# Optimization experiments

Hardware: AMD Instinct MI355X
Metric: run time of the kernel (lower is better)

The kernel has to match this reference:

```python
import jax, jax.numpy as jnp
import numpy as np

B, N, H, D, DEPTH = 16, 1024, 2, 128, 3
A = H * D  # atten_dim = 256
FFN = 1024
EPS = 1e-5


def layer_norm(x, g, b):
    mu = jnp.mean(x, axis=-1, keepdims=True)
    var = jnp.mean(jnp.square(x - mu), axis=-1, keepdims=True)
    return (x - mu) * jax.lax.rsqrt(var + EPS) * g + b


def setup_inputs() -> dict:
    key = jax.random.key(0)
    ks = jax.random.split(key, 16)
    s = lambda fan_in: 1.0 / np.sqrt(fan_in)
    inp = {
        "X": jax.random.normal(ks[0], (B, N, A), jnp.float32),
        # per-layer attention projections, stacked over depth
        "Wq": jax.random.normal(ks[1], (DEPTH, A, A), jnp.float32) * s(A),
        "bq": jnp.zeros((DEPTH, A), jnp.float32),
        "Wk": jax.random.normal(ks[2], (DEPTH, A, A), jnp.float32) * s(A),
        "bk": jnp.zeros((DEPTH, A), jnp.float32),
        "Wv": jax.random.normal(ks[3], (DEPTH, A, A), jnp.float32) * s(A),
        "bv": jnp.zeros((DEPTH, A), jnp.float32),
        # per-layer FFN (roll_out): Linear(A,1024)+ReLU, Linear(1024,A)+ReLU
        "W1": jax.random.normal(ks[4], (DEPTH, A, FFN), jnp.float32) * s(A),
        "b1": jnp.zeros((DEPTH, FFN), jnp.float32),
        "W2": jax.random.normal(ks[5], (DEPTH, FFN, A), jnp.float32) * s(FFN),
        "b2": jnp.zeros((DEPTH, A), jnp.float32),
        # single shared LayerNorm (the torch module reuses one instance)
        "ln_g": jnp.ones((A,), jnp.float32),
        "ln_b": jnp.zeros((A,), jnp.float32),
        # Conv1d(A, A, kernel_size=1) == per-position linear over channels
        "Wc": jax.random.normal(ks[6], (A, A), jnp.float32) * s(A),
        "bc": jnp.zeros((A,), jnp.float32),
        # final Linear(A, A) on pooled features
        "We": jax.random.normal(ks[7], (A, A), jnp.float32) * s(A),
        "be": jnp.zeros((A,), jnp.float32),
    }
    return inp


def reference(X, Wq, bq, Wk, bk, Wv, bv, W1, b1, W2, b2, ln_g, ln_b, Wc, bc, We, be):
    inv_sqrt_d = 1.0 / np.sqrt(D)
    step = X  # [B, N, A]
    for i in range(DEPTH):
        q = (step @ Wq[i] + bq[i]).reshape(B, N, H, D).transpose(0, 2, 1, 3)
        k = (step @ Wk[i] + bk[i]).reshape(B, N, H, D).transpose(0, 2, 1, 3)
        v = (step @ Wv[i] + bv[i]).reshape(B, N, H, D).transpose(0, 2, 1, 3)
        scores = jnp.einsum('bhqd,bhkd->bhqk', q, k) * inv_sqrt_d
        probs = jax.nn.softmax(scores, axis=-1)
        attn = jnp.einsum('bhqk,bhkd->bhqd', probs, v)
        attn = attn.transpose(0, 2, 1, 3).reshape(B, N, A)
        roll = jax.nn.relu(jax.nn.relu(attn @ W1[i] + b1[i]) @ W2[i] + b2[i])
        step = layer_norm(roll + step, ln_g, ln_b)
    # Conv1d(kernel=1) + ReLU over channels, per position
    entity_encodings = jax.nn.relu(step @ Wc + bc)  # [B, N, A]
    pooled = jnp.mean(entity_encodings, axis=1)      # [B, A]
    encoded_entities = jax.nn.relu(pooled @ We + be)  # [B, A]
    return encoded_entities
```

## Files before the change

### kernel.cpp

```cpp
#include <hip/hip_runtime.h>
#include <hip/hip_bf16.h>
#include <cstddef>

#define B_   16
#define N_   1024
#define H_   2
#define D_   128
#define A_   256
#define FFN_ 1024
#define M_   (B_ * N_)
#define EPS_ 1e-5f
#define SPLIT 4
#define KT   32
#define TPC  (N_ / SPLIT / KT)
#define QKV_E ((size_t)B_ * H_ * N_ * D_)

typedef short  short8  __attribute__((ext_vector_type(8)));
typedef float  f32x16  __attribute__((ext_vector_type(16)));
typedef unsigned int uint;
typedef unsigned short ushort;

#define MFMA32(a, b, c) __builtin_amdgcn_mfma_f32_32x32x16_bf16(a, b, c, 0, 0, 0)

__device__ __forceinline__ uint f2b1(float x) {
    uint u = __float_as_uint(x);
    return (u + 0x7fffu + ((u >> 16) & 1u)) >> 16;
}
__device__ __forceinline__ uint f2b2(float lo, float hi) {
    return f2b1(lo) | (f2b1(hi) << 16);
}
__device__ __forceinline__ float b2f(ushort u) {
    return __uint_as_float(((uint)u) << 16);
}

__global__ __launch_bounds__(256) void f32_to_bf16_kernel(
    const float* __restrict__ in, ushort* __restrict__ out)
{
    const size_t i = ((size_t)blockIdx.x * 256 + threadIdx.x) * 8;
    float4 a = *(const float4*)(in + i);
    float4 b = *(const float4*)(in + i + 4);
    uint4 w = { f2b2(a.x, a.y), f2b2(a.z, a.w), f2b2(b.x, b.y), f2b2(b.z, b.w) };
    *(uint4*)(out + i) = w;
}

__global__ __launch_bounds__(256) void transpose_bf16_kernel(
    const float* __restrict__ W, ushort* __restrict__ Wt, int K, int N,
    size_t sstride, size_t dstride)
{
    __shared__ float tile[32][33];
    W  += (size_t)blockIdx.z * sstride;
    Wt += (size_t)blockIdx.z * dstride;
    const int n0 = blockIdx.x * 32, k0 = blockIdx.y * 32;
    const int tc = threadIdx.x & 31, tr = threadIdx.x >> 5;
#pragma unroll
    for (int it = 0; it < 4; ++it) {
        int r = it * 8 + tr;
        tile[r][tc] = W[(size_t)(k0 + r) * N + n0 + tc];
    }
    __syncthreads();
#pragma unroll
    for (int it = 0; it < 4; ++it) {
        int r = it * 8 + tr;
        Wt[(size_t)(n0 + r) * K + k0 + tc] = (ushort)f2b1(tile[tc][r]);
    }
}

__global__ __launch_bounds__(256) void transpose_qkv_kernel(
    const float* __restrict__ Wq, const float* __restrict__ Wk,
    const float* __restrict__ Wv, ushort* __restrict__ dst)
{
    __shared__ float tile[32][33];
    const int layer = blockIdx.z / 3, sec = blockIdx.z % 3;
    const float* W = (sec == 0 ? Wq : sec == 1 ? Wk : Wv) + (size_t)layer * A_ * A_;
    ushort* out = dst + (size_t)layer * (3 * A_ * A_) + (size_t)sec * A_ * A_;
    const int n0 = blockIdx.x * 32, k0 = blockIdx.y * 32;
    const int tc = threadIdx.x & 31, tr = threadIdx.x >> 5;
#pragma unroll
    for (int it = 0; it < 4; ++it) {
        int r = it * 8 + tr;
        tile[r][tc] = W[(size_t)(k0 + r) * A_ + n0 + tc];
    }
    __syncthreads();
#pragma unroll
    for (int it = 0; it < 4; ++it) {
        int r = it * 8 + tr;
        out[(size_t)(n0 + r) * A_ + k0 + tc] = (ushort)f2b1(tile[tc][r]);
    }
}

template <int MR>
__global__ __launch_bounds__(256) void gemm_mfma(
    const ushort* __restrict__ Asrc, const ushort* __restrict__ Wt,
    const float* __restrict__ bias, const float* __restrict__ biasK,
    const float* __restrict__ biasV, void* __restrict__ outp,
    int K, int ldc, int mode)
{
    constexpr int BM = MR * 64;
    __shared__ ushort sA[BM * 72];
    __shared__ ushort sB[128 * 72];

    const int tid = threadIdx.x;
    const int wid = tid >> 6, lane = tid & 63;
    const int c = lane & 31, g = lane >> 5;
    const int wr = wid >> 1, wc = wid & 1;
    const int m0 = blockIdx.x * BM;
    const int n0 = blockIdx.y * 128;

    f32x16 acc[MR][2] = {};

    for (int k0 = 0; k0 < K; k0 += 64) {
        __syncthreads();
#pragma unroll
        for (int it = 0; it < BM / 32; ++it) {
            int idx = it * 256 + tid, r = idx >> 3, cc = (idx & 7) * 8;
            *(uint4*)&sA[r * 72 + cc] =
                *(const uint4*)(Asrc + (size_t)(m0 + r) * K + k0 + cc);
        }
#pragma unroll
        for (int it = 0; it < 4; ++it) {
            int idx = it * 256 + tid, r = idx >> 3, cc = (idx & 7) * 8;
            *(uint4*)&sB[r * 72 + cc] =
                *(const uint4*)(Wt + (size_t)(n0 + r) * K + k0 + cc);
        }
        __syncthreads();
#pragma unroll
        for (int ks = 0; ks < 4; ++ks) {
            const int ko = ks * 16 + 8 * g;
            short8 b0 = *(const short8*)&sB[(wc * 64 + c) * 72 + ko];
            short8 b1 = *(const short8*)&sB[(wc * 64 + 32 + c) * 72 + ko];
#pragma unroll
            for (int mr = 0; mr < MR; ++mr) {
                short8 a = *(const short8*)&sA[((wr * MR + mr) * 32 + c) * 72 + ko];
                acc[mr][0] = MFMA32(a, b0, acc[mr][0]);
                acc[mr][1] = MFMA32(a, b1, acc[mr][1]);
            }
        }
    }

    const int sec = n0 >> 8;
    const float* bp = bias;
    int nw = n0;
    if (mode == 5) {
        bp = (sec == 0 ? bias : sec == 1 ? biasK : biasV);
        nw = n0 & 255;
    }
    const float bz[2] = { bp[nw + wc * 64 + c], bp[nw + wc * 64 + 32 + c] };

    float colsum[2] = { 0.f, 0.f };

#pragma unroll
    for (int mr = 0; mr < MR; ++mr) {
#pragma unroll
        for (int ct = 0; ct < 2; ++ct) {
            const int colbase = n0 + wc * 64 + ct * 32 + c;
#pragma unroll
            for (int rg = 0; rg < 4; ++rg) {
                const int row = m0 + (wr * MR + mr) * 32 + 8 * rg + 4 * g;
                float v0 = acc[mr][ct][4 * rg + 0] + bz[ct];
                float v1 = acc[mr][ct][4 * rg + 1] + bz[ct];
                float v2 = acc[mr][ct][4 * rg + 2] + bz[ct];
                float v3 = acc[mr][ct][4 * rg + 3] + bz[ct];
                if (mode == 1 || mode == 2 || mode == 6) {
                    v0 = fmaxf(v0, 0.f); v1 = fmaxf(v1, 0.f);
                    v2 = fmaxf(v2, 0.f); v3 = fmaxf(v3, 0.f);
                }
                if (mode == 1) {
                    float* o = (float*)outp;
                    o[(size_t)(row + 0) * ldc + colbase] = v0;
                    o[(size_t)(row + 1) * ldc + colbase] = v1;
                    o[(size_t)(row + 2) * ldc + colbase] = v2;
                    o[(size_t)(row + 3) * ldc + colbase] = v3;
                } else if (mode == 2) {
                    ushort* o = (ushort*)outp;
                    o[(size_t)(row + 0) * ldc + colbase] = (ushort)f2b1(v0);
                    o[(size_t)(row + 1) * ldc + colbase] = (ushort)f2b1(v1);
                    o[(size_t)(row + 2) * ldc + colbase] = (ushort)f2b1(v2);
                    o[(size_t)(row + 3) * ldc + colbase] = (ushort)f2b1(v3);
                } else if (mode == 6) {
                    colsum[ct] += v0 + v1 + v2 + v3;
                } else {
                    const int cw = colbase & 255;
                    const int hh = cw >> 7, dd = cw & (D_ - 1);
                    if (sec < 2) {
                        ushort* o = (ushort*)outp + (size_t)sec * QKV_E;
#pragma unroll
                        for (int r2 = 0; r2 < 4; ++r2) {
                            int rw = row + r2;
                            int bb = rw >> 10, np = rw & (N_ - 1);
                            float vv = (r2 == 0 ? v0 : r2 == 1 ? v1 : r2 == 2 ? v2 : v3);
                            size_t off = (((size_t)(bb * H_ + hh) * 32 + (np >> 5)) * 16
                                          + (dd >> 3)) * 256
                                         + (np & 31) * 8 + (dd & 7);
                            o[off] = (ushort)f2b1(vv);
                        }
                    } else {
                        ushort* o = (ushort*)outp + 2 * QKV_E;
                        const int bb = row >> 10, np = row & (N_ - 1);
                        size_t off = ((((size_t)(bb * H_ + hh) * 32 + (np >> 5)) * 4
                                       + (dd >> 5)) * 4 + ((np & 31) >> 3)) * 256
                                     + (dd & 31) * 8 + (np & 7);
                        uint2 w = { f2b2(v0, v1), f2b2(v2, v3) };
                        *(uint2*)(o + off) = w;
                    }
                }
            }
        }
    }

    if (mode == 6) {
        float* part = (float*)outp;
        const int b = m0 >> 10;
#pragma unroll
        for (int ct = 0; ct < 2; ++ct) {
            float cs = colsum[ct] + __shfl_xor(colsum[ct], 32, 64);
            if (g == 0)
                atomicAdd(&part[(size_t)b * A_ + n0 + wc * 64 + ct * 32 + c], cs);
        }
    }
}

#define OPITCH 132

__global__ __launch_bounds__(128, 3) void attn_kernel(
    const ushort* __restrict__ qg, const ushort* __restrict__ kg,
    const ushort* __restrict__ vtg, ushort* __restrict__ po,
    float* __restrict__ pm, float* __restrict__ pl)
{
    __shared__ ushort sO[64 * OPITCH];

    const int tid = threadIdx.x;
    const int w = tid >> 6, lane = tid & 63;
    const int c = lane & 31, g = lane >> 5;

    const int flat = blockIdx.x;
    const int xcd  = flat & 7;
    const int ii   = flat >> 3;
    const int pair = xcd * 16 + (ii & 15);
    const int qt   = ii >> 4;
    const int bh   = pair & 31;
    const int z    = pair >> 5;

    const int q0 = qt * 64 + w * 32;
    const float scale2 = 0.08838834764831845f * 1.44269504f;
    const float THR = 11.5f;
    const int lo8 = c * 8;

    short8 qf[8];
    const ushort* qt_ = qg + ((size_t)bh * 32 + (q0 >> 5)) * 4096;
#pragma unroll
    for (int ks = 0; ks < 8; ++ks)
        qf[ks] = *(const short8*)(qt_ + (2 * ks + g) * 256 + lo8);

    f32x16 oacc[4] = {};
    float m = -1e30f, l = 0.f;

    for (int t = 0; t < TPC; ++t) {
        const size_t tb = ((size_t)bh * 32 + z * 8 + t) * 4096;
        const ushort* kt_ = kg + tb;
        const ushort* vt_ = vtg + tb;

        f32x16 sacc = {};
        __builtin_amdgcn_s_setprio(1);
#pragma unroll
        for (int ks = 0; ks < 8; ++ks) {
            short8 a = *(const short8*)(kt_ + (2 * ks + g) * 256 + lo8);
            sacc = MFMA32(a, qf[ks], sacc);
        }
        __builtin_amdgcn_s_setprio(0);

        float p[16];
        float tmax = -1e30f;
#pragma unroll
        for (int r = 0; r < 16; ++r) {
            float s = sacc[r] * scale2;
            p[r] = s;
            tmax = fmaxf(tmax, s);
        }
        tmax = fmaxf(tmax, __shfl_xor(tmax, 32, 64));
        if (!__all(tmax - m <= THR)) {
            const float mnew = fmaxf(m, tmax);
            const float corr = exp2f(m - mnew);
#pragma unroll
            for (int dt = 0; dt < 4; ++dt)
#pragma unroll
                for (int r = 0; r < 16; ++r) oacc[dt][r] *= corr;
            l *= corr;
            m = mnew;
        }
        float tsum = 0.f;
#pragma unroll
        for (int r = 0; r < 16; ++r) {
            p[r] = exp2f(p[r] - m);
            tsum += p[r];
        }
        tsum += __shfl_xor(tsum, 32, 64);
        l += tsum;

        uint pk[8];
#pragma unroll
        for (int pp = 0; pp < 8; ++pp)
            pk[pp] = f2b2(p[2 * pp], p[2 * pp + 1]);

        uint v0 = g ? pk[0] : pk[2];
        uint v1 = g ? pk[1] : pk[3];
        uint v2 = g ? pk[4] : pk[6];
        uint v3 = g ? pk[5] : pk[7];
        uint r0 = (uint)__shfl_xor((int)v0, 32, 64);
        uint r1 = (uint)__shfl_xor((int)v1, 32, 64);
        uint r2 = (uint)__shfl_xor((int)v2, 32, 64);
        uint r3 = (uint)__shfl_xor((int)v3, 32, 64);

        __builtin_amdgcn_s_setprio(1);
#pragma unroll
        for (int kb = 0; kb < 2; ++kb) {
            union { uint u[4]; short8 s; } pf;
            if (kb == 0) {
                pf.u[0] = g ? r0 : pk[0];
                pf.u[1] = g ? r1 : pk[1];
                pf.u[2] = g ? pk[2] : r0;
                pf.u[3] = g ? pk[3] : r1;
            } else {
                pf.u[0] = g ? r2 : pk[4];
                pf.u[1] = g ? r3 : pk[5];
                pf.u[2] = g ? pk[6] : r2;
                pf.u[3] = g ? pk[7] : r3;
            }
#pragma unroll
            for (int dt = 0; dt < 4; ++dt) {
                short8 a = *(const short8*)(vt_ + dt * 1024 + kb * 512 + g * 256 + lo8);
                oacc[dt] = MFMA32(a, pf.s, oacc[dt]);
            }
        }
        __builtin_amdgcn_s_setprio(0);
    }

    if (lane < 32) {
        pm[(size_t)(z * 32 + bh) * N_ + q0 + c] = m;
        pl[(size_t)(z * 32 + bh) * N_ + q0 + c] = l;
    }
    {
        const int qrl = w * 32 + c;
#pragma unroll
        for (int dt = 0; dt < 4; ++dt)
#pragma unroll
            for (int rg = 0; rg < 4; ++rg) {
                int d = dt * 32 + 8 * rg + 4 * g;
                uint2 pv = { f2b2(oacc[dt][4 * rg + 0], oacc[dt][4 * rg + 1]),
                             f2b2(oacc[dt][4 * rg + 2], oacc[dt][4 * rg + 3]) };
                *(uint2*)&sO[qrl * OPITCH + d] = pv;
            }
    }
    __syncthreads();
    {
        const size_t pbase = ((size_t)(z * 32 + bh) * N_ + qt * 64) * D_;
#pragma unroll
        for (int it = 0; it < 16; ++it) {
            int idx = it * 128 + tid;
            int r = idx >> 5, dgr = (idx & 31) * 4;
            uint2 v = *(const uint2*)&sO[r * OPITCH + dgr];
            *(uint2*)(po + pbase + (size_t)r * D_ + dgr) = v;
        }
    }
}

__global__ __launch_bounds__(256) void combine_kernel(
    const ushort* __restrict__ po, const float* __restrict__ pm,
    const float* __restrict__ pl, ushort* __restrict__ out)
{
    const int idx = blockIdx.x * 256 + threadIdx.x;
    const int row = idx >> 4, d0 = (idx & 15) * 8;
    const int R = B_ * H_ * N_;

    float ms[SPLIT];
    float M = -1e30f;
#pragma unroll
    for (int s = 0; s < SPLIT; ++s) {
        ms[s] = pm[(size_t)s * R + row];
        M = fmaxf(M, ms[s]);
    }
    float L = 0.f;
    float acc[8] = {};
#pragma unroll
    for (int s = 0; s < SPLIT; ++s) {
        float wgt = exp2f(ms[s] - M);
        L += pl[(size_t)s * R + row] * wgt;
        uint4 pv = *(const uint4*)(po + ((size_t)s * R + row) * D_ + d0);
        const ushort* pu = (const ushort*)&pv;
#pragma unroll
        for (int j = 0; j < 8; ++j) acc[j] += b2f(pu[j]) * wgt;
    }
    const float inv = 1.f / L;
    uint4 w;
    w.x = f2b2(acc[0] * inv, acc[1] * inv);
    w.y = f2b2(acc[2] * inv, acc[3] * inv);
    w.z = f2b2(acc[4] * inv, acc[5] * inv);
    w.w = f2b2(acc[6] * inv, acc[7] * inv);
    const int bh = row >> 10, n = row & (N_ - 1);
    const int bb = bh >> 1, hh = bh & 1;
    *(uint4*)(out + ((size_t)(bb * N_ + n)) * A_ + hh * D_ + d0) = w;
}

__global__ __launch_bounds__(256) void add_ln_kernel(
    const ushort* __restrict__ roll, const float* __restrict__ prev,
    const float* __restrict__ g, const float* __restrict__ bta,
    float* __restrict__ out, ushort* __restrict__ outb)
{
    const int row = blockIdx.x * 4 + (threadIdx.x >> 6);
    const int lane = threadIdx.x & 63, c4 = lane * 4;
    const size_t base = (size_t)row * A_ + c4;

    uint2 rb = *(const uint2*)(roll + base);
    float4 pv = *(const float4*)(prev + base);
    float v0 = b2f((ushort)(rb.x & 0xffff)) + pv.x;
    float v1 = b2f((ushort)(rb.x >> 16))    + pv.y;
    float v2 = b2f((ushort)(rb.y & 0xffff)) + pv.z;
    float v3 = b2f((ushort)(rb.y >> 16))    + pv.w;

    float s  = v0 + v1 + v2 + v3;
    float s2 = v0 * v0 + v1 * v1 + v2 * v2 + v3 * v3;
#pragma unroll
    for (int o = 32; o > 0; o >>= 1) {
        s  += __shfl_xor(s, o, 64);
        s2 += __shfl_xor(s2, o, 64);
    }
    const float mu = s * (1.f / A_);
    const float rs = rsqrtf(s2 * (1.f / A_) - mu * mu + EPS_);

    float4 gv = *(const float4*)(g + c4);
    float4 bv = *(const float4*)(bta + c4);
    float y0 = (v0 - mu) * rs * gv.x + bv.x;
    float y1 = (v1 - mu) * rs * gv.y + bv.y;
    float y2 = (v2 - mu) * rs * gv.z + bv.z;
    float y3 = (v3 - mu) * rs * gv.w + bv.w;

    float4 yo = { y0, y1, y2, y3 };
    *(float4*)(out + base) = yo;
    uint2 yb = { f2b2(y0, y1), f2b2(y2, y3) };
    *(uint2*)(outb + base) = yb;
}

__global__ __launch_bounds__(256) void final_kernel(
    const float* __restrict__ part, const float* __restrict__ We,
    const float* __restrict__ be, float* __restrict__ out)
{
    __shared__ float sp[A_];
    const int b = blockIdx.x, tid = threadIdx.x;
    sp[tid] = part[(size_t)b * A_ + tid] * (1.0f / N_);
    __syncthreads();
    float acc = be[tid];
    for (int kk = 0; kk < A_; ++kk) acc += sp[kk] * We[(size_t)kk * A_ + tid];
    out[b * A_ + tid] = fmaxf(acc, 0.f);
}

extern "C" void kernel_launch(void* const* d_in, const int* in_sizes, int n_in,
                              void* d_out, int out_size, void* d_ws, size_t ws_size,
                              hipStream_t stream)
{
    const float* X    = (const float*)d_in[0];
    const float* Wq   = (const float*)d_in[1];
    const float* bq   = (const float*)d_in[2];
    const float* Wk   = (const float*)d_in[3];
    const float* bk   = (const float*)d_in[4];
    const float* Wv   = (const float*)d_in[5];
    const float* bv   = (const float*)d_in[6];
    const float* W1   = (const float*)d_in[7];
    const float* b1   = (const float*)d_in[8];
    const float* W2   = (const float*)d_in[9];
    const float* b2   = (const float*)d_in[10];
    const float* ln_g = (const float*)d_in[11];
    const float* ln_b = (const float*)d_in[12];
    const float* Wc   = (const float*)d_in[13];
    const float* bc   = (const float*)d_in[14];
    const float* We   = (const float*)d_in[15];
    const float* be   = (const float*)d_in[16];

    char* base = (char*)d_ws;
    ushort* qb     = (ushort*)base;  base += QKV_E * 2;
                             base += QKV_E * 2;
                             base += QKV_E * 2;
    ushort* hbuf   = (ushort*)base;  base += (size_t)M_ * FFN_ * 2;
    ushort* rollb  = (ushort*)base;  base += (size_t)M_ * A_ * 2;
    float*  step   = (float*)base;   base += (size_t)M_ * A_ * 4;
    ushort* stepb  = (ushort*)base;  base += (size_t)M_ * A_ * 2;
    ushort* wqkv_t = (ushort*)base;  base += (size_t)3 * 3 * A_ * A_ * 2;
    ushort* w1_t   = (ushort*)base;  base += (size_t)3 * A_ * FFN_ * 2;
    ushort* w2_t   = (ushort*)base;  base += (size_t)3 * FFN_ * A_ * 2;
    ushort* wc_t   = (ushort*)base;  base += (size_t)A_ * A_ * 2;
    float*  part   = (float*)base;   base += (size_t)B_ * A_ * 4;
    float*  pm     = (float*)base;   base += (size_t)SPLIT * B_ * H_ * N_ * 4;
    float*  pl     = (float*)base;   base += (size_t)SPLIT * B_ * H_ * N_ * 4;
    ushort* kbuf   = qb + QKV_E;
    ushort* vtbuf  = qb + 2 * QKV_E;
    ushort* po     = hbuf;
    ushort* attnb  = qb;

    transpose_qkv_kernel<<<dim3(8, 8, 9), 256, 0, stream>>>(Wq, Wk, Wv, wqkv_t);
    transpose_bf16_kernel<<<dim3(FFN_/32, A_/32, 3), 256, 0, stream>>>(
        W1, w1_t, A_, FFN_, (size_t)A_ * FFN_, (size_t)A_ * FFN_);
    transpose_bf16_kernel<<<dim3(A_/32, FFN_/32, 3), 256, 0, stream>>>(
        W2, w2_t, FFN_, A_, (size_t)FFN_ * A_, (size_t)FFN_ * A_);
    transpose_bf16_kernel<<<dim3(A_/32, A_/32, 1), 256, 0, stream>>>(
        Wc, wc_t, A_, A_, 0, 0);
    f32_to_bf16_kernel<<<(M_ * A_) / (256 * 8), 256, 0, stream>>>(X, stepb);

    const float* cur = X;
    for (int i = 0; i < 3; ++i) {
        gemm_mfma<2><<<dim3(M_/128, 6), 256, 0, stream>>>(
            stepb, wqkv_t + (size_t)i * 3 * A_ * A_,
            bq + i * A_, bk + i * A_, bv + i * A_, qb, A_, 0, 5);

        attn_kernel<<<16 * SPLIT * B_ * H_, 128, 0, stream>>>(
            qb, kbuf, vtbuf, po, pm, pl);
        combine_kernel<<<(B_*H_*N_*D_)/(256*8), 256, 0, stream>>>(po, pm, pl, attnb);

        gemm_mfma<2><<<dim3(M_/128, FFN_/128), 256, 0, stream>>>(
            attnb, w1_t + (size_t)i * A_ * FFN_, b1 + i * FFN_, nullptr, nullptr,
            hbuf, A_, FFN_, 2);
        gemm_mfma<1><<<dim3(M_/64, A_/128), 256, 0, stream>>>(
            hbuf, w2_t + (size_t)i * FFN_ * A_, b2 + i * A_, nullptr, nullptr,
            rollb, FFN_, A_, 2);

        add_ln_kernel<<<M_/4, 256, 0, stream>>>(rollb, cur, ln_g, ln_b, step, stepb);
        cur = step;
    }

    hipMemsetAsync(part, 0, (size_t)B_ * A_ * 4, stream);
    gemm_mfma<1><<<dim3(M_/64, A_/128), 256, 0, stream>>>(
        stepb, wc_t, bc, nullptr, nullptr, part, A_, 0, 6);
    final_kernel<<<B_, 256, 0, stream>>>(part, We, be, (float*)d_out);
}
```

Measured before the change: 402.2 us.

## Merge weight-prep launches, prefetch V fragments early, raise attention occupancy

Folds the four weight transpose/convert launches into a single prep kernel indexed by blockIdx.z, which removes three kernel launches. The attention kernel now loads all eight V fragments right after the QK MFMAs and places a sched_barrier, so the V loads can overlap the softmax work. It also raises the launch_bounds minimum from 3 to 4 blocks per CU. The extra live V registers, combined with the tighter register cap, risk spills.

New measurement: 450.4 us. 12.0% more time.

```diff
diff --git a/kernel.cpp b/kernel.cpp
--- a/kernel.cpp
+++ b/kernel.cpp
@@ -43,14 +43,38 @@
     *(uint4*)(out + i) = w;
 }
 
-__global__ __launch_bounds__(256) void transpose_bf16_kernel(
-    const float* __restrict__ W, ushort* __restrict__ Wt, int K, int N,
-    size_t sstride, size_t dstride)
-{
+__global__ __launch_bounds__(256) void prep_kernel(
+    const float* __restrict__ Wq, const float* __restrict__ Wk,
+    const float* __restrict__ Wv, const float* __restrict__ W1,
+    const float* __restrict__ W2, const float* __restrict__ Wc,
+    ushort* __restrict__ wqkv_t, ushort* __restrict__ w1_t,
+    ushort* __restrict__ w2_t, ushort* __restrict__ wc_t)
+{
+    const int z = blockIdx.z;
+    const float* W; ushort* out; int K, N, n0, k0;
+    if (z < 9) {
+        const int layer = z / 3, sec = z % 3;
+        W = (sec == 0 ? Wq : sec == 1 ? Wk : Wv) + (size_t)layer * A_ * A_;
+        out = wqkv_t + (size_t)layer * 3 * A_ * A_ + (size_t)sec * A_ * A_;
+        K = A_; N = A_;
+        n0 = blockIdx.x * 32; k0 = blockIdx.y * 32;
+    } else if (z < 12) {
+        const int layer = z - 9;
+        W = W1 + (size_t)layer * A_ * FFN_; out = w1_t + (size_t)layer * A_ * FFN_;
+        K = A_; N = FFN_;
+        n0 = blockIdx.x * 32; k0 = blockIdx.y * 32;
+    } else if (z < 15) {
+        const int layer = z - 12;
+        W = W2 + (size_t)layer * FFN_ * A_; out = w2_t + (size_t)layer * FFN_ * A_;
+        K = FFN_; N = A_;
+        k0 = blockIdx.x * 32; n0 = blockIdx.y * 32;
+    } else {
+        W = Wc; out = wc_t; K = A_; N = A_;
+        n0 = blockIdx.x * 32; k0 = blockIdx.y * 32;
+    }
+    if (n0 >= N || k0 >= K) return;
+
     __shared__ float tile[32][33];
-    W  += (size_t)blockIdx.z * sstride;
-    Wt += (size_t)blockIdx.z * dstride;
-    const int n0 = blockIdx.x * 32, k0 = blockIdx.y * 32;
     const int tc = threadIdx.x & 31, tr = threadIdx.x >> 5;
 #pragma unroll
     for (int it = 0; it < 4; ++it) {
@@ -61,30 +85,7 @@
 #pragma unroll
     for (int it = 0; it < 4; ++it) {
         int r = it * 8 + tr;
-        Wt[(size_t)(n0 + r) * K + k0 + tc] = (ushort)f2b1(tile[tc][r]);
-    }
-}
-
-__global__ __launch_bounds__(256) void transpose_qkv_kernel(
-    const float* __restrict__ Wq, const float* __restrict__ Wk,
-    const float* __restrict__ Wv, ushort* __restrict__ dst)
-{
-    __shared__ float tile[32][33];
-    const int layer = blockIdx.z / 3, sec = blockIdx.z % 3;
-    const float* W = (sec == 0 ? Wq : sec == 1 ? Wk : Wv) + (size_t)layer * A_ * A_;
-    ushort* out = dst + (size_t)layer * (3 * A_ * A_) + (size_t)sec * A_ * A_;
-    const int n0 = blockIdx.x * 32, k0 = blockIdx.y * 32;
-    const int tc = threadIdx.x & 31, tr = threadIdx.x >> 5;
-#pragma unroll
-    for (int it = 0; it < 4; ++it) {
-        int r = it * 8 + tr;
-        tile[r][tc] = W[(size_t)(k0 + r) * A_ + n0 + tc];
-    }
-    __syncthreads();
-#pragma unroll
-    for (int it = 0; it < 4; ++it) {
-        int r = it * 8 + tr;
-        out[(size_t)(n0 + r) * A_ + k0 + tc] = (ushort)f2b1(tile[tc][r]);
+        out[(size_t)(n0 + r) * K + k0 + tc] = (ushort)f2b1(tile[tc][r]);
     }
 }
 
@@ -221,7 +222,7 @@
 
 #define OPITCH 132
 
-__global__ __launch_bounds__(128, 3) void attn_kernel(
+__global__ __launch_bounds__(128, 4) void attn_kernel(
     const ushort* __restrict__ qg, const ushort* __restrict__ kg,
     const ushort* __restrict__ vtg, ushort* __restrict__ po,
     float* __restrict__ pm, float* __restrict__ pl)
@@ -267,6 +268,17 @@
             sacc = MFMA32(a, qf[ks], sacc);
         }
         __builtin_amdgcn_s_setprio(0);
+
+        const ushort* vb = vt_ + g * 256 + lo8;
+        short8 vfA0 = *(const short8*)(vb + 0 * 1024);
+        short8 vfA1 = *(const short8*)(vb + 1 * 1024);
+        short8 vfA2 = *(const short8*)(vb + 2 * 1024);
+        short8 vfA3 = *(const short8*)(vb + 3 * 1024);
+        short8 vfB0 = *(const short8*)(vb + 0 * 1024 + 512);
+        short8 vfB1 = *(const short8*)(vb + 1 * 1024 + 512);
+        short8 vfB2 = *(const short8*)(vb + 2 * 1024 + 512);
+        short8 vfB3 = *(const short8*)(vb + 3 * 1024 + 512);
+        __builtin_amdgcn_sched_barrier(0);
 
         float p[16];
         float tmax = -1e30f;
@@ -325,11 +337,10 @@
                 pf.u[2] = g ? pk[6] : r2;
                 pf.u[3] = g ? pk[7] : r3;
             }
-#pragma unroll
-            for (int dt = 0; dt < 4; ++dt) {
-                short8 a = *(const short8*)(vt_ + dt * 1024 + kb * 512 + g * 256 + lo8);
-                oacc[dt] = MFMA32(a, pf.s, oacc[dt]);
-            }
+            oacc[0] = MFMA32(kb ? vfB0 : vfA0, pf.s, oacc[0]);
+            oacc[1] = MFMA32(kb ? vfB1 : vfA1, pf.s, oacc[1]);
+            oacc[2] = MFMA32(kb ? vfB2 : vfA2, pf.s, oacc[2]);
+            oacc[3] = MFMA32(kb ? vfB3 : vfA3, pf.s, oacc[3]);
         }
         __builtin_amdgcn_s_setprio(0);
     }
@@ -494,13 +505,8 @@
     ushort* po     = hbuf;
     ushort* attnb  = qb;
 
-    transpose_qkv_kernel<<<dim3(8, 8, 9), 256, 0, stream>>>(Wq, Wk, Wv, wqkv_t);
-    transpose_bf16_kernel<<<dim3(FFN_/32, A_/32, 3), 256, 0, stream>>>(
-        W1, w1_t, A_, FFN_, (size_t)A_ * FFN_, (size_t)A_ * FFN_);
-    transpose_bf16_kernel<<<dim3(A_/32, FFN_/32, 3), 256, 0, stream>>>(
-        W2, w2_t, FFN_, A_, (size_t)FFN_ * A_, (size_t)FFN_ * A_);
-    transpose_bf16_kernel<<<dim3(A_/32, A_/32, 1), 256, 0, stream>>>(
-        Wc, wc_t, A_, A_, 0, 0);
+    prep_kernel<<<dim3(32, 8, 16), 256, 0, stream>>>(
+        Wq, Wk, Wv, W1, W2, Wc, wqkv_t, w1_t, w2_t, wc_t);
     f32_to_bf16_kernel<<<(M_ * A_) / (256 * 8), 256, 0, stream>>>(X, stepb);
 
     const float* cur = X;
```
